# Performance work log

Measured on AMD Instinct MI355X. Metric: run time of the kernel, lower is better.

The kernel has to match this reference:

```python
import jax, jax.numpy as jnp
import numpy as np

N, E, D_IN, HID, HEADS, D_OUT, R = 20000, 640000, 256, 128, 4, 128, 32
NEG_SLOPE = 0.2  # PyG GATConv default


def setup_inputs() -> dict:
    key = jax.random.key(0)
    ks = jax.random.split(key, 12)
    s = 0.05
    return {
        "x": jax.random.normal(ks[0], (N, D_IN), jnp.float32),
        "edge_index": jax.random.randint(ks[1], (2, E), 0, N, dtype=jnp.int64),
        "edge_type": jax.random.randint(ks[2], (E,), 0, R, dtype=jnp.int64),
        "rel_emb": jax.random.normal(ks[3], (R, D_IN), jnp.float32) * s,
        "W1": jax.random.normal(ks[4], (D_IN, HEADS * HID), jnp.float32) * s,
        "att_src1": jax.random.normal(ks[5], (HEADS, HID), jnp.float32) * s,
        "att_dst1": jax.random.normal(ks[6], (HEADS, HID), jnp.float32) * s,
        "b1": jnp.zeros((HEADS * HID,), jnp.float32),
        "W2": jax.random.normal(ks[7], (HEADS * HID, D_OUT), jnp.float32) * s,
        "att_src2": jax.random.normal(ks[8], (1, D_OUT), jnp.float32) * s,
        "att_dst2": jax.random.normal(ks[9], (1, D_OUT), jnp.float32) * s,
        "b2": jnp.zeros((D_OUT,), jnp.float32),
    }


def _gat_conv(x, src, dst, W, a_src, a_dst, bias, heads, ch):
    """PyG GATConv (eval mode, self loops already in src/dst)."""
    n = x.shape[0]
    h = (x @ W).reshape(n, heads, ch)                      # [N,H,C]
    alpha_s = jnp.einsum('nhc,hc->nh', h, a_src)           # [N,H]
    alpha_d = jnp.einsum('nhc,hc->nh', h, a_dst)
    e = jax.nn.leaky_relu(alpha_s[src] + alpha_d[dst], NEG_SLOPE)  # [E,H]
    # segment softmax over incoming edges of each dst node
    m = jax.ops.segment_max(e, dst, num_segments=n)        # [N,H]
    p = jnp.exp(e - m[dst])
    denom = jax.ops.segment_sum(p, dst, num_segments=n)
    alpha = p / (denom[dst] + 1e-16)                       # [E,H]
    out = jax.ops.segment_sum(h[src] * alpha[:, :, None], dst, num_segments=n)
    return out.reshape(n, heads * ch) + bias


def reference(x, edge_index, edge_type, rel_emb, W1, att_src1, att_dst1, b1,
              W2, att_src2, att_dst2, b2):
    src, dst = edge_index[0], edge_index[1]
    # relational feature injection: x_mod[src] += rel_emb[edge_type]
    x_mod = x.at[src].add(rel_emb[edge_type])
    # GATConv adds self loops by default
    loop = jnp.arange(N, dtype=src.dtype)
    s2 = jnp.concatenate([src, loop])
    d2 = jnp.concatenate([dst, loop])
    h = _gat_conv(x_mod, s2, d2, W1, att_src1, att_dst1, b1, HEADS, HID)
    h = jax.nn.elu(h)
    return _gat_conv(h, s2, d2, W2, att_src2, att_dst2, b2, 1, D_OUT)
```

## Files before the change

### kernel.cpp

```cpp
#include <hip/hip_runtime.h>


#define D_IN   256
#define HID1   512
#define NHEADS 4
#define DOUT   128
#define NREL   32
#define NEG_SLOPE 0.2f
#define M_PAD  20096

static __device__ __forceinline__ unsigned short f2b(float f) {
  union { float f; unsigned int i; } v; v.f = f;
  unsigned int x = v.i;
  return (unsigned short)((x + 0x7fffu + ((x >> 16) & 1u)) >> 16);
}
static __device__ __forceinline__ float lrelu(float x) {
  return x > 0.f ? x : NEG_SLOPE * x;
}

typedef __attribute__((ext_vector_type(8))) short bf16x8;
typedef __attribute__((ext_vector_type(4))) float f32x4;
typedef __attribute__((ext_vector_type(2))) float f32x2;

static __device__ __forceinline__ f32x2 up2(unsigned int u) {
  union { unsigned int i; float f; } lo, hi;
  lo.i = u << 16; hi.i = u & 0xffff0000u;
  f32x2 v; v.x = lo.f; v.y = hi.f; return v;
}
static __device__ __forceinline__ void accp(f32x2* acc, float w, uint4 r) {
  f32x2 wv = (f32x2)(w);
  acc[0] += wv * up2(r.x);
  acc[1] += wv * up2(r.y);
  acc[2] += wv * up2(r.z);
  acc[3] += wv * up2(r.w);
}

__global__ void prep_kernel(const int* __restrict__ src, const int* __restrict__ dst,
                            const int* __restrict__ et, int* __restrict__ counts,
                            int* __restrict__ deg, int E, int eb, int cb,
                            const float* __restrict__ W1, const float* __restrict__ W2,
                            unsigned short* __restrict__ W1T, unsigned short* __restrict__ W2T,
                            const float* __restrict__ att_s1, const float* __restrict__ att_d1,
                            float* __restrict__ us4, float* __restrict__ ud4,
                            const float* __restrict__ att_s2, const float* __restrict__ att_d2,
                            float* __restrict__ vs, float* __restrict__ vd) {
  int b = blockIdx.x;
  int t = threadIdx.x;
  if (b < eb) {
    int e = b * 256 + t;
    if (e >= E) return;
    atomicAdd(&counts[(size_t)src[e] * NREL + et[e]], 1);
    atomicAdd(&deg[dst[e]], 1);
  } else if (b < eb + cb) {
    int idx = (b - eb) * 256 + t;
    if (idx < D_IN * HID1) {
      int r = idx / HID1, c = idx % HID1;
      W1T[(size_t)c * D_IN + r] = f2b(W1[idx]);
    } else {
      int k = idx - D_IN * HID1;
      if (k < HID1 * DOUT) {
        int r = k / DOUT, c = k % DOUT;
        W2T[(size_t)c * HID1 + r] = f2b(W2[k]);
      }
    }
  } else if (b == eb + cb) {
    int k = t;
    float us[4] = {0.f, 0.f, 0.f, 0.f}, ud[4] = {0.f, 0.f, 0.f, 0.f};
    for (int h = 0; h < 4; ++h)
      for (int c = 0; c < 128; ++c) {
        float wv = W1[(size_t)k * HID1 + h * 128 + c];
        us[h] += wv * att_s1[h * 128 + c];
        ud[h] += wv * att_d1[h * 128 + c];
      }
    ((float4*)us4)[k] = make_float4(us[0], us[1], us[2], us[3]);
    ((float4*)ud4)[k] = make_float4(ud[0], ud[1], ud[2], ud[3]);
  } else {
#pragma unroll
    for (int rr = 0; rr < 2; ++rr) {
      int r = t * 2 + rr;
      float ss = 0.f, dd = 0.f;
      for (int c = 0; c < DOUT; ++c) {
        float wv = W2[(size_t)r * DOUT + c];
        ss += wv * att_s2[c];
        dd += wv * att_d2[c];
      }
      vs[r] = ss; vd[r] = dd;
    }
  }
}

__global__ void scan_local(const int* __restrict__ in, int* __restrict__ out,
                           int* __restrict__ bsum, int n) {
  __shared__ int wsum[4];
  int t = threadIdx.x;
  int base = blockIdx.x * 1024 + t * 4;
  int v0 = (base + 0 < n) ? in[base + 0] : 0;
  int v1 = (base + 1 < n) ? in[base + 1] : 0;
  int v2 = (base + 2 < n) ? in[base + 2] : 0;
  int v3 = (base + 3 < n) ? in[base + 3] : 0;
  int s = v0 + v1 + v2 + v3;
  int lane = t & 63, w = t >> 6;
  int sc = s;
  for (int off = 1; off < 64; off <<= 1) {
    int u = __shfl_up(sc, off);
    if (lane >= off) sc += u;
  }
  if (lane == 63) wsum[w] = sc;
  __syncthreads();
  int woff = 0;
  for (int i = 0; i < w; ++i) woff += wsum[i];
  int excl = woff + sc - s;
  if (base + 0 < n) out[base + 0] = excl;
  if (base + 1 < n) out[base + 1] = excl + v0;
  if (base + 2 < n) out[base + 2] = excl + v0 + v1;
  if (base + 3 < n) out[base + 3] = excl + v0 + v1 + v2;
  if (t == 255) bsum[blockIdx.x] = woff + sc;
}

__global__ void scan_blocks(int* __restrict__ bsum, int nb,
                            int* __restrict__ offsets, int n) {
  int t = threadIdx.x;
  int v = (t < nb) ? bsum[t] : 0;
  int sc = v;
  for (int off = 1; off < 64; off <<= 1) {
    int u = __shfl_up(sc, off);
    if (t >= off) sc += u;
  }
  if (t < nb) bsum[t] = sc - v;
  if (t == nb - 1) offsets[n] = v;
}

__global__ void scatter_kernel(const int* __restrict__ src, const int* __restrict__ dst,
                               const int* __restrict__ offsets, const int* __restrict__ bsum,
                               int* __restrict__ cursor, int* __restrict__ csr_src, int E) {
  int e = blockIdx.x * 256 + threadIdx.x;
  if (e >= E) return;
  int d = dst[e];
  int pos = offsets[d] + bsum[d >> 10] + atomicAdd(&cursor[d], 1);
  csr_src[pos] = src[e];
}

__global__ __launch_bounds__(256) void xmod_kernel(
    const float* __restrict__ x, const int* __restrict__ counts,
    const float* __restrict__ rel, const float* __restrict__ us4,
    const float* __restrict__ ud4, unsigned short* __restrict__ x_modb,
    float* __restrict__ as1, float* __restrict__ ad1, int n_nodes) {
  int wv = threadIdx.x >> 6;
  int node = blockIdx.x * 4 + wv;
  if (node >= n_nodes) return;
  int l = threadIdx.x & 63;
  int cnt_l = counts[(size_t)node * NREL + (l & 31)];
  const float4* x4 = (const float4*)x;
  const float4* rel4 = (const float4*)rel;
  float4 v = x4[(size_t)node * 64 + l];
#pragma unroll
  for (int r = 0; r < NREL; ++r) {
    int c = __shfl(cnt_l, r);
    if (c) {
      float4 rv = rel4[r * 64 + l];
      float fc = (float)c;
      v.x += fc * rv.x; v.y += fc * rv.y; v.z += fc * rv.z; v.w += fc * rv.w;
    }
  }
  ushort4 o;
  o.x = f2b(v.x); o.y = f2b(v.y); o.z = f2b(v.z); o.w = f2b(v.w);
  *(ushort4*)(x_modb + (size_t)node * D_IN + l * 4) = o;
  const float4* usv = (const float4*)us4;
  const float4* udv = (const float4*)ud4;
  float vv[4] = {v.x, v.y, v.z, v.w};
  float sh[4] = {0.f, 0.f, 0.f, 0.f}, dh[4] = {0.f, 0.f, 0.f, 0.f};
#pragma unroll
  for (int i = 0; i < 4; ++i) {
    float4 uu = usv[l * 4 + i];
    float4 dd = udv[l * 4 + i];
    sh[0] += vv[i] * uu.x; sh[1] += vv[i] * uu.y; sh[2] += vv[i] * uu.z; sh[3] += vv[i] * uu.w;
    dh[0] += vv[i] * dd.x; dh[1] += vv[i] * dd.y; dh[2] += vv[i] * dd.z; dh[3] += vv[i] * dd.w;
  }
  for (int off = 32; off; off >>= 1) {
#pragma unroll
    for (int h = 0; h < 4; ++h) {
      sh[h] += __shfl_xor(sh[h], off);
      dh[h] += __shfl_xor(dh[h], off);
    }
  }
  if (l == 0) {
    ((float4*)as1)[node] = make_float4(sh[0], sh[1], sh[2], sh[3]);
    ((float4*)ad1)[node] = make_float4(dh[0], dh[1], dh[2], dh[3]);
  }
}

__global__ __launch_bounds__(256) void aggregate1_kernel(
    const unsigned short* __restrict__ x_modb,
    const float* __restrict__ as1, const float* __restrict__ ad1,
    const int* __restrict__ offsets, const int* __restrict__ bsum,
    const int* __restrict__ csr_src,
    unsigned short* __restrict__ agg_xb, int n_nodes) {
  int node = blockIdx.x * 4 + (threadIdx.x >> 6);
  if (node >= n_nodes) return;
  int lane = threadIdx.x & 63;
  int hp = lane >> 5, l32 = lane & 31;
  int lo = offsets[node] + bsum[node >> 10];
  int hi = offsets[node + 1] + bsum[(node + 1) >> 10];
  float2 adp = *(const float2*)(ad1 + (size_t)node * 4 + 2 * hp);
  float2 asp = *(const float2*)(as1 + (size_t)node * 4 + 2 * hp);

  const uint4* xv = (const uint4*)x_modb;
  f32x2 acc0[4], acc1[4];
#pragma unroll
  for (int k = 0; k < 4; ++k) { acc0[k] = (f32x2)(0.f); acc1[k] = (f32x2)(0.f); }
  f32x2 den = (f32x2)(0.f);

  int n_it = hi - lo;
  int j = lo;
  int s = (j < hi) ? csr_src[j] : node;
  float2 av = *(const float2*)(as1 + (size_t)s * 4 + 2 * hp);
  for (int i = 0; i < n_it; ++i) {
    int jn = j + 1;
    int sn = (jn < hi) ? csr_src[jn] : node;
    float2 avn = *(const float2*)(as1 + (size_t)sn * 4 + 2 * hp);
    uint4 r = xv[(size_t)s * 32 + l32];
    float w0 = __expf(lrelu(av.x + adp.x));
    float w1 = __expf(lrelu(av.y + adp.y));
    accp(acc0, w0, r);
    accp(acc1, w1, r);
    den.x += w0; den.y += w1;
    j = jn; s = sn; av = avn;
  }
  {
    uint4 r = xv[(size_t)node * 32 + l32];
    float w0 = __expf(lrelu(asp.x + adp.x));
    float w1 = __expf(lrelu(asp.y + adp.y));
    accp(acc0, w0, r);
    accp(acc1, w1, r);
    den.x += w0; den.y += w1;
  }
  float inv0 = 1.f / (den.x + 1e-16f);
  float inv1 = 1.f / (den.y + 1e-16f);
  unsigned int od0[4], od1[4];
#pragma unroll
  for (int p = 0; p < 4; ++p) {
    od0[p] = (unsigned int)f2b(acc0[p].x * inv0) | ((unsigned int)f2b(acc0[p].y * inv0) << 16);
    od1[p] = (unsigned int)f2b(acc1[p].x * inv1) | ((unsigned int)f2b(acc1[p].y * inv1) << 16);
  }
  uint4 o0; o0.x = od0[0]; o0.y = od0[1]; o0.z = od0[2]; o0.w = od0[3];
  uint4 o1; o1.x = od1[0]; o1.y = od1[1]; o1.z = od1[2]; o1.w = od1[3];
  *(uint4*)(agg_xb + ((size_t)(2 * hp) * M_PAD + node) * D_IN + l32 * 8) = o0;
  *(uint4*)(agg_xb + ((size_t)(2 * hp + 1) * M_PAD + node) * D_IN + l32 * 8) = o1;
}

template <int BM, int MODE>
__global__ __launch_bounds__(256) void mfma_gemm(
    const unsigned short* __restrict__ A, const unsigned short* __restrict__ BT,
    unsigned short* __restrict__ C, int M, int N, int K,
    const float* __restrict__ bias, const float* __restrict__ vs,
    const float* __restrict__ vd, float* __restrict__ as2, float* __restrict__ ad2) {
  constexpr int MFR = BM / 32;
  __shared__ __align__(16) unsigned short Asl[BM * 32];
  __shared__ __align__(16) unsigned short Bsl[128 * 32];
  int tid = threadIdx.x;
  int m0 = blockIdx.y * BM, n0 = blockIdx.x * 128;
  int lane = tid & 63, wv = tid >> 6;
  int wm = wv & 1, wn = wv >> 1;
  int l16 = lane & 15, quad = lane >> 4;
  int lr = lane >> 2, lseg = lane & 3;
  if (MODE == 1) A += (size_t)blockIdx.x * M_PAD * K;

  f32x4 acc[MFR][4];
#pragma unroll
  for (int i = 0; i < MFR; ++i)
#pragma unroll
    for (int j = 0; j < 4; ++j) acc[i][j] = (f32x4)(0.f);

  for (int k0 = 0; k0 < K; k0 += 32) {
#pragma unroll
    for (int c = wv; c < BM / 16; c += 4) {
      int gr = m0 + c * 16 + lr; gr = gr < M ? gr : M - 1;
      __builtin_amdgcn_global_load_lds(
          (const __attribute__((address_space(1))) void*)(A + (size_t)gr * K + k0 + lseg * 8),
          (__attribute__((address_space(3))) void*)(&Asl[c * 512]), 16, 0, 0);
    }
#pragma unroll
    for (int c = wv; c < 8; c += 4) {
      int gr = n0 + c * 16 + lr;
      __builtin_amdgcn_global_load_lds(
          (const __attribute__((address_space(1))) void*)(BT + (size_t)gr * K + k0 + lseg * 8),
          (__attribute__((address_space(3))) void*)(&Bsl[c * 512]), 16, 0, 0);
    }
    __syncthreads();
    bf16x8 af[MFR], bfr[4];
#pragma unroll
    for (int mf = 0; mf < MFR; ++mf)
      af[mf] = *(const bf16x8*)(&Asl[(wm * (BM / 2) + mf * 16 + l16) * 32 + quad * 8]);
#pragma unroll
    for (int nf = 0; nf < 4; ++nf)
      bfr[nf] = *(const bf16x8*)(&Bsl[(wn * 64 + nf * 16 + l16) * 32 + quad * 8]);
#pragma unroll
    for (int mf = 0; mf < MFR; ++mf)
#pragma unroll
      for (int nf = 0; nf < 4; ++nf)
        acc[mf][nf] = __builtin_amdgcn_mfma_f32_16x16x32_bf16(af[mf], bfr[nf], acc[mf][nf], 0, 0, 0);
    __syncthreads();
  }
  if (MODE == 0) {
#pragma unroll
    for (int mf = 0; mf < MFR; ++mf)
#pragma unroll
      for (int nf = 0; nf < 4; ++nf)
#pragma unroll
        for (int r = 0; r < 4; ++r) {
          int row = m0 + wm * (BM / 2) + mf * 16 + quad * 4 + r;
          int col = n0 + wn * 64 + nf * 16 + l16;
          C[(size_t)row * N + col] = f2b(acc[mf][nf][r]);
        }
  } else {
#pragma unroll
    for (int mf = 0; mf < MFR; ++mf)
#pragma unroll
      for (int r = 0; r < 4; ++r) {
        int row = m0 + wm * (BM / 2) + mf * 16 + quad * 4 + r;
        float sd = 0.f, dd = 0.f;
#pragma unroll
        for (int nf = 0; nf < 4; ++nf) {
          int col = n0 + wn * 64 + nf * 16 + l16;
          float cv = acc[mf][nf][r] + bias[col];
          cv = cv > 0.f ? cv : expm1f(cv);
          C[(size_t)row * N + col] = f2b(cv);
          sd += cv * vs[col];
          dd += cv * vd[col];
        }
#pragma unroll
        for (int off = 1; off < 16; off <<= 1) {
          sd += __shfl_xor(sd, off);
          dd += __shfl_xor(dd, off);
        }
        if (l16 == 0 && row < M) {
          atomicAdd(&as2[row], sd);
          atomicAdd(&ad2[row], dd);
        }
      }
  }
}

__global__ __launch_bounds__(256) void aggregate2_kernel(
    const unsigned short* __restrict__ t2b,
    const float* __restrict__ as2, const float* __restrict__ ad2,
    const int* __restrict__ offsets, const int* __restrict__ bsum,
    const int* __restrict__ csr_src,
    const float* __restrict__ bias, float* __restrict__ out, int n_nodes) {
  int node = blockIdx.x * 4 + (threadIdx.x >> 6);
  if (node >= n_nodes) return;
  int lane = threadIdx.x & 63;
  int g = lane >> 4, l16 = lane & 15;
  int lo = offsets[node] + bsum[node >> 10];
  int hi = offsets[node + 1] + bsum[(node + 1) >> 10];
  float ad = ad2[node];

  const uint4* t2v = (const uint4*)t2b;
  f32x2 acc[4];
#pragma unroll
  for (int k = 0; k < 4; ++k) acc[k] = (f32x2)(0.f);
  float denom = 0.f;
  int nit = (hi - lo + 3) >> 2;
  int j = lo + g;
  bool valid = j < hi;
  int s = valid ? csr_src[j] : node;
  float asv = as2[s];
  for (int i = 0; i < nit; ++i) {
    int jn = j + 4;
    bool vn = jn < hi;
    int sn = vn ? csr_src[jn] : node;
    float asv_n = as2[sn];
    uint4 tv = t2v[(size_t)s * 16 + l16];
    float w = valid ? __expf(lrelu(asv + ad)) : 0.f;
    accp(acc, w, tv);
    denom += w;
    j = jn; valid = vn; s = sn; asv = asv_n;
  }
  if (g == 0) {
    uint4 tv = t2v[(size_t)node * 16 + l16];
    float w = __expf(lrelu(as2[node] + ad));
    accp(acc, w, tv);
    denom += w;
  }
#pragma unroll
  for (int k = 0; k < 4; ++k) {
    acc[k].x += __shfl_xor(acc[k].x, 16); acc[k].y += __shfl_xor(acc[k].y, 16);
    acc[k].x += __shfl_xor(acc[k].x, 32); acc[k].y += __shfl_xor(acc[k].y, 32);
  }
  denom += __shfl_xor(denom, 16);
  denom += __shfl_xor(denom, 32);
  if (g == 0) {
    float inv = 1.f / (denom + 1e-16f);
    float4 o0, o1;
    o0.x = acc[0].x * inv + bias[l16 * 8 + 0];
    o0.y = acc[0].y * inv + bias[l16 * 8 + 1];
    o0.z = acc[1].x * inv + bias[l16 * 8 + 2];
    o0.w = acc[1].y * inv + bias[l16 * 8 + 3];
    o1.x = acc[2].x * inv + bias[l16 * 8 + 4];
    o1.y = acc[2].y * inv + bias[l16 * 8 + 5];
    o1.z = acc[3].x * inv + bias[l16 * 8 + 6];
    o1.w = acc[3].y * inv + bias[l16 * 8 + 7];
    *(float4*)(out + (size_t)node * DOUT + l16 * 8) = o0;
    *(float4*)(out + (size_t)node * DOUT + l16 * 8 + 4) = o1;
  }
}

extern "C" void kernel_launch(void* const* d_in, const int* in_sizes, int n_in,
                              void* d_out, int out_size, void* d_ws, size_t ws_size,
                              hipStream_t stream) {
  const float* x     = (const float*)d_in[0];
  const int* ei      = (const int*)d_in[1];
  const int* etype   = (const int*)d_in[2];
  const float* rel   = (const float*)d_in[3];
  const float* W1    = (const float*)d_in[4];
  const float* at_s1 = (const float*)d_in[5];
  const float* at_d1 = (const float*)d_in[6];
  const float* b1    = (const float*)d_in[7];
  const float* W2    = (const float*)d_in[8];
  const float* at_s2 = (const float*)d_in[9];
  const float* at_d2 = (const float*)d_in[10];
  const float* b2v   = (const float*)d_in[11];
  float* out         = (float*)d_out;

  const int N = in_sizes[0] / D_IN;
  const int E = in_sizes[2];
  const int* srcv = ei;
  const int* dstv = ei + E;

  char* p = (char*)d_ws;
  auto carve = [&](size_t bytes) -> char* {
    char* r = p; p += (bytes + 255) & ~(size_t)255; return r;
  };
  int*   counts  = (int*)carve((size_t)N * NREL * 4);
  int*   deg     = (int*)carve((size_t)N * 4);
  int*   offsets = (int*)carve(((size_t)N + 1) * 4);
  int*   cursor  = (int*)carve((size_t)N * 4);
  int*   bsum    = (int*)carve(64 * 4);
  float* as2     = (float*)carve((size_t)N * 4);
  float* ad2     = (float*)carve((size_t)N * 4);
  size_t zero_bytes = (size_t)(p - (char*)counts);
  float* as1     = (float*)carve((size_t)N * NHEADS * 4);
  float* ad1     = (float*)carve((size_t)N * NHEADS * 4);
  float* vs      = (float*)carve((size_t)HID1 * 4);
  float* vd      = (float*)carve((size_t)HID1 * 4);
  float* us4     = (float*)carve((size_t)D_IN * 4 * 4);
  float* ud4     = (float*)carve((size_t)D_IN * 4 * 4);
  int*   csr_src = (int*)carve((size_t)E * 4);
  unsigned short* W1T    = (unsigned short*)carve((size_t)HID1 * D_IN * 2);
  unsigned short* W2T    = (unsigned short*)carve((size_t)DOUT * HID1 * 2);
  unsigned short* x_modb = (unsigned short*)carve((size_t)N * D_IN * 2);
  unsigned short* agg_xb = (unsigned short*)carve((size_t)NHEADS * M_PAD * D_IN * 2);
  unsigned short* h2b    = (unsigned short*)carve((size_t)M_PAD * HID1 * 2);
  unsigned short* t2b    = (unsigned short*)carve((size_t)M_PAD * DOUT * 2);

  hipMemsetAsync(counts, 0, zero_bytes, stream);

  int eb = (E + 255) / 256;
  int cb = (D_IN * HID1 + HID1 * DOUT + 255) / 256;
  int nb = (N + 1023) / 1024;
  prep_kernel<<<eb + cb + 2, 256, 0, stream>>>(srcv, dstv, etype, counts, deg, E, eb, cb,
                                               W1, W2, W1T, W2T, at_s1, at_d1, us4, ud4,
                                               at_s2, at_d2, vs, vd);
  scan_local<<<nb, 256, 0, stream>>>(deg, offsets, bsum, N);
  scan_blocks<<<1, 64, 0, stream>>>(bsum, nb, offsets, N);
  scatter_kernel<<<eb, 256, 0, stream>>>(srcv, dstv, offsets, bsum, cursor, csr_src, E);
  xmod_kernel<<<(N + 3) / 4, 256, 0, stream>>>(x, counts, rel, us4, ud4, x_modb, as1, ad1, N);
  aggregate1_kernel<<<(N + 3) / 4, 256, 0, stream>>>(x_modb, as1, ad1, offsets, bsum,
                                                     csr_src, agg_xb, N);
  mfma_gemm<128, 1><<<dim3(NHEADS, M_PAD / 128), 256, 0, stream>>>(
      agg_xb, W1T, h2b, N, HID1, D_IN, b1, vs, vd, as2, ad2);
  mfma_gemm<64, 0><<<dim3(DOUT / 128, M_PAD / 64), 256, 0, stream>>>(
      h2b, W2T, t2b, N, DOUT, HID1, nullptr, nullptr, nullptr, nullptr, nullptr);
  aggregate2_kernel<<<(N + 3) / 4, 256, 0, stream>>>(
      t2b, as2, ad2, offsets, bsum, csr_src, b2v, out, N);
}
```

Measured before the change: 344.1 us.

## Build CSR with per-block LDS histograms and restructure layer-1 aggregation loop

Replaces global-atomic degree counting and scatter with 128 blocks that each build an LDS histogram of destinations, followed by column-sum, rebase and LDS-cursor scatter kernels. Packs relation counts into 8-bit fields to shrink the counts buffer and its atomics. Rewrites aggregate1 so each half-wave handles alternate edges for all four heads using packed FMA asm with a prefetch of the next row, and adds row prefetching to aggregate2. Risks: 8-bit counts overflow if a node has more than 255 edges of one relation, the new scatter order is deterministic but extra kernel launches are added, and the gtable aliases the h2b buffer.

```diff
diff --git a/kernel.cpp b/kernel.cpp
--- a/kernel.cpp
+++ b/kernel.cpp
@@ -8,6 +8,7 @@
 #define NREL   32
 #define NEG_SLOPE 0.2f
 #define M_PAD  20096
+#define NB     128
 
 static __device__ __forceinline__ unsigned short f2b(float f) {
   union { float f; unsigned int i; } v; v.f = f;
@@ -27,32 +28,67 @@
   lo.i = u << 16; hi.i = u & 0xffff0000u;
   f32x2 v; v.x = lo.f; v.y = hi.f; return v;
 }
+static __device__ __forceinline__ void pkfma(f32x2& a, f32x2 b, f32x2 c) {
+  asm("v_pk_fma_f32 %0, %1, %2, %0" : "+v"(a) : "v"(b), "v"(c));
+}
 static __device__ __forceinline__ void accp(f32x2* acc, float w, uint4 r) {
   f32x2 wv = (f32x2)(w);
-  acc[0] += wv * up2(r.x);
-  acc[1] += wv * up2(r.y);
-  acc[2] += wv * up2(r.z);
-  acc[3] += wv * up2(r.w);
-}
-
-__global__ void prep_kernel(const int* __restrict__ src, const int* __restrict__ dst,
-                            const int* __restrict__ et, int* __restrict__ counts,
-                            int* __restrict__ deg, int E, int eb, int cb,
-                            const float* __restrict__ W1, const float* __restrict__ W2,
-                            unsigned short* __restrict__ W1T, unsigned short* __restrict__ W2T,
-                            const float* __restrict__ att_s1, const float* __restrict__ att_d1,
-                            float* __restrict__ us4, float* __restrict__ ud4,
-                            const float* __restrict__ att_s2, const float* __restrict__ att_d2,
-                            float* __restrict__ vs, float* __restrict__ vd) {
+  pkfma(acc[0], wv, up2(r.x));
+  pkfma(acc[1], wv, up2(r.y));
+  pkfma(acc[2], wv, up2(r.z));
+  pkfma(acc[3], wv, up2(r.w));
+}
+static __device__ __forceinline__ void acc4(f32x2 acc[4][4], float* den,
+                                            float4 av, float4 adv, uint4 r) {
+  float w0 = __expf(lrelu(av.x + adv.x));
+  float w1 = __expf(lrelu(av.y + adv.y));
+  float w2 = __expf(lrelu(av.z + adv.z));
+  float w3 = __expf(lrelu(av.w + adv.w));
+  f32x2 x0 = up2(r.x), x1 = up2(r.y), x2 = up2(r.z), x3 = up2(r.w);
+  f32x2 wv;
+  wv = (f32x2)(w0);
+  pkfma(acc[0][0], wv, x0); pkfma(acc[0][1], wv, x1);
+  pkfma(acc[0][2], wv, x2); pkfma(acc[0][3], wv, x3);
+  wv = (f32x2)(w1);
+  pkfma(acc[1][0], wv, x0); pkfma(acc[1][1], wv, x1);
+  pkfma(acc[1][2], wv, x2); pkfma(acc[1][3], wv, x3);
+  wv = (f32x2)(w2);
+  pkfma(acc[2][0], wv, x0); pkfma(acc[2][1], wv, x1);
+  pkfma(acc[2][2], wv, x2); pkfma(acc[2][3], wv, x3);
+  wv = (f32x2)(w3);
+  pkfma(acc[3][0], wv, x0); pkfma(acc[3][1], wv, x1);
+  pkfma(acc[3][2], wv, x2); pkfma(acc[3][3], wv, x3);
+  den[0] += w0; den[1] += w1; den[2] += w2; den[3] += w3;
+}
+
+__global__ __launch_bounds__(256) void hist_prep_kernel(
+    const int* __restrict__ src, const int* __restrict__ dst,
+    const int* __restrict__ et, unsigned int* __restrict__ counts8,
+    int* __restrict__ gtable, int E, int n, int cb,
+    const float* __restrict__ W1, const float* __restrict__ W2,
+    unsigned short* __restrict__ W1T, unsigned short* __restrict__ W2T,
+    const float* __restrict__ att_s1, const float* __restrict__ att_d1,
+    float* __restrict__ us4, float* __restrict__ ud4,
+    const float* __restrict__ att_s2, const float* __restrict__ att_d2,
+    float* __restrict__ vs, float* __restrict__ vd) {
   int b = blockIdx.x;
   int t = threadIdx.x;
-  if (b < eb) {
-    int e = b * 256 + t;
-    if (e >= E) return;
-    atomicAdd(&counts[(size_t)src[e] * NREL + et[e]], 1);
-    atomicAdd(&deg[dst[e]], 1);
-  } else if (b < eb + cb) {
-    int idx = (b - eb) * 256 + t;
+  if (b < NB) {
+    extern __shared__ int hist[];
+    for (int i = t; i < n; i += 256) hist[i] = 0;
+    __syncthreads();
+    int per = (E + NB - 1) / NB;
+    int e0 = b * per;
+    int e1 = min(e0 + per, E);
+    for (int e = e0 + t; e < e1; e += 256) {
+      atomicAdd(&hist[dst[e]], 1);
+      int s = src[e], r = et[e];
+      atomicAdd(&counts8[(size_t)s * 8 + (r >> 2)], 1u << (8 * (r & 3)));
+    }
+    __syncthreads();
+    for (int i = t; i < n; i += 256) gtable[(size_t)b * n + i] = hist[i];
+  } else if (b < NB + cb) {
+    int idx = (b - NB) * 256 + t;
     if (idx < D_IN * HID1) {
       int r = idx / HID1, c = idx % HID1;
       W1T[(size_t)c * D_IN + r] = f2b(W1[idx]);
@@ -63,7 +99,7 @@
         W2T[(size_t)c * HID1 + r] = f2b(W2[k]);
       }
     }
-  } else if (b == eb + cb) {
+  } else if (b == NB + cb) {
     int k = t;
     float us[4] = {0.f, 0.f, 0.f, 0.f}, ud[4] = {0.f, 0.f, 0.f, 0.f};
     for (int h = 0; h < 4; ++h)
@@ -87,6 +123,16 @@
       vs[r] = ss; vd[r] = dd;
     }
   }
+}
+
+__global__ void colsum_kernel(const int* __restrict__ gtable,
+                              int* __restrict__ deg, int n) {
+  int d = blockIdx.x * 256 + threadIdx.x;
+  if (d >= n) return;
+  int s = 0;
+#pragma unroll 8
+  for (int b = 0; b < NB; ++b) s += gtable[(size_t)b * n + d];
+  deg[d] = s;
 }
 
 __global__ void scan_local(const int* __restrict__ in, int* __restrict__ out,
@@ -130,18 +176,39 @@
   if (t == nb - 1) offsets[n] = v;
 }
 
-__global__ void scatter_kernel(const int* __restrict__ src, const int* __restrict__ dst,
-                               const int* __restrict__ offsets, const int* __restrict__ bsum,
-                               int* __restrict__ cursor, int* __restrict__ csr_src, int E) {
-  int e = blockIdx.x * 256 + threadIdx.x;
-  if (e >= E) return;
-  int d = dst[e];
-  int pos = offsets[d] + bsum[d >> 10] + atomicAdd(&cursor[d], 1);
-  csr_src[pos] = src[e];
+__global__ void rebase_kernel(int* __restrict__ gtable,
+                              const int* __restrict__ offsets,
+                              const int* __restrict__ bsum, int n) {
+  int d = blockIdx.x * 256 + threadIdx.x;
+  if (d >= n) return;
+  int run = offsets[d] + bsum[d >> 10];
+  for (int b = 0; b < NB; ++b) {
+    size_t idx = (size_t)b * n + d;
+    int v = gtable[idx];
+    gtable[idx] = run;
+    run += v;
+  }
+}
+
+__global__ __launch_bounds__(256) void scatter2_kernel(
+    const int* __restrict__ src, const int* __restrict__ dst,
+    const int* __restrict__ gtable, int* __restrict__ csr_src, int E, int n) {
+  extern __shared__ int cur[];
+  int b = blockIdx.x;
+  int t = threadIdx.x;
+  for (int i = t; i < n; i += 256) cur[i] = gtable[(size_t)b * n + i];
+  __syncthreads();
+  int per = (E + NB - 1) / NB;
+  int e0 = b * per;
+  int e1 = min(e0 + per, E);
+  for (int e = e0 + t; e < e1; e += 256) {
+    int pos = atomicAdd(&cur[dst[e]], 1);
+    csr_src[pos] = src[e];
+  }
 }
 
 __global__ __launch_bounds__(256) void xmod_kernel(
-    const float* __restrict__ x, const int* __restrict__ counts,
+    const float* __restrict__ x, const unsigned int* __restrict__ counts8,
     const float* __restrict__ rel, const float* __restrict__ us4,
     const float* __restrict__ ud4, unsigned short* __restrict__ x_modb,
     float* __restrict__ as1, float* __restrict__ ad1, int n_nodes) {
@@ -149,7 +216,9 @@
   int node = blockIdx.x * 4 + wv;
   if (node >= n_nodes) return;
   int l = threadIdx.x & 63;
-  int cnt_l = counts[(size_t)node * NREL + (l & 31)];
+  int r5 = l & 31;
+  unsigned int cw = counts8[(size_t)node * 8 + (r5 >> 2)];
+  int cnt_l = (int)((cw >> (8 * (r5 & 3))) & 0xffu);
   const float4* x4 = (const float4*)x;
   const float4* rel4 = (const float4*)rel;
   float4 v = x4[(size_t)node * 64 + l];
@@ -198,54 +267,58 @@
   int node = blockIdx.x * 4 + (threadIdx.x >> 6);
   if (node >= n_nodes) return;
   int lane = threadIdx.x & 63;
-  int hp = lane >> 5, l32 = lane & 31;
+  int half = lane >> 5, l32 = lane & 31;
   int lo = offsets[node] + bsum[node >> 10];
   int hi = offsets[node + 1] + bsum[(node + 1) >> 10];
-  float2 adp = *(const float2*)(ad1 + (size_t)node * 4 + 2 * hp);
-  float2 asp = *(const float2*)(as1 + (size_t)node * 4 + 2 * hp);
-
+  float4 adv = ((const float4*)ad1)[node];
   const uint4* xv = (const uint4*)x_modb;
-  f32x2 acc0[4], acc1[4];
-#pragma unroll
-  for (int k = 0; k < 4; ++k) { acc0[k] = (f32x2)(0.f); acc1[k] = (f32x2)(0.f); }
-  f32x2 den = (f32x2)(0.f);
-
-  int n_it = hi - lo;
-  int j = lo;
+  const float4* as1v = (const float4*)as1;
+
+  f32x2 acc[4][4];
+#pragma unroll
+  for (int h = 0; h < 4; ++h)
+#pragma unroll
+    for (int k = 0; k < 4; ++k) acc[h][k] = (f32x2)(0.f);
+  float den[4] = {0.f, 0.f, 0.f, 0.f};
+
+  int j = lo + half;
   int s = (j < hi) ? csr_src[j] : node;
-  float2 av = *(const float2*)(as1 + (size_t)s * 4 + 2 * hp);
-  for (int i = 0; i < n_it; ++i) {
-    int jn = j + 1;
+  float4 av = as1v[(unsigned)s];
+  uint4 r = xv[(unsigned)((s << 5) | l32)];
+  while (j < hi) {
+    int jn = j + 2;
     int sn = (jn < hi) ? csr_src[jn] : node;
-    float2 avn = *(const float2*)(as1 + (size_t)sn * 4 + 2 * hp);
-    uint4 r = xv[(size_t)s * 32 + l32];
-    float w0 = __expf(lrelu(av.x + adp.x));
-    float w1 = __expf(lrelu(av.y + adp.y));
-    accp(acc0, w0, r);
-    accp(acc1, w1, r);
-    den.x += w0; den.y += w1;
-    j = jn; s = sn; av = avn;
-  }
-  {
-    uint4 r = xv[(size_t)node * 32 + l32];
-    float w0 = __expf(lrelu(asp.x + adp.x));
-    float w1 = __expf(lrelu(asp.y + adp.y));
-    accp(acc0, w0, r);
-    accp(acc1, w1, r);
-    den.x += w0; den.y += w1;
-  }
-  float inv0 = 1.f / (den.x + 1e-16f);
-  float inv1 = 1.f / (den.y + 1e-16f);
-  unsigned int od0[4], od1[4];
-#pragma unroll
-  for (int p = 0; p < 4; ++p) {
-    od0[p] = (unsigned int)f2b(acc0[p].x * inv0) | ((unsigned int)f2b(acc0[p].y * inv0) << 16);
-    od1[p] = (unsigned int)f2b(acc1[p].x * inv1) | ((unsigned int)f2b(acc1[p].y * inv1) << 16);
-  }
-  uint4 o0; o0.x = od0[0]; o0.y = od0[1]; o0.z = od0[2]; o0.w = od0[3];
-  uint4 o1; o1.x = od1[0]; o1.y = od1[1]; o1.z = od1[2]; o1.w = od1[3];
-  *(uint4*)(agg_xb + ((size_t)(2 * hp) * M_PAD + node) * D_IN + l32 * 8) = o0;
-  *(uint4*)(agg_xb + ((size_t)(2 * hp + 1) * M_PAD + node) * D_IN + l32 * 8) = o1;
+    float4 avn = as1v[(unsigned)sn];
+    uint4 rn = xv[(unsigned)((sn << 5) | l32)];
+    acc4(acc, den, av, adv, r);
+    j = jn; s = sn; av = avn; r = rn;
+  }
+  if (half == 0) {
+    float4 asv = as1v[(unsigned)node];
+    uint4 rs = xv[(unsigned)((node << 5) | l32)];
+    acc4(acc, den, asv, adv, rs);
+  }
+#pragma unroll
+  for (int h = 0; h < 4; ++h) {
+#pragma unroll
+    for (int k = 0; k < 4; ++k) {
+      acc[h][k].x += __shfl_xor(acc[h][k].x, 32);
+      acc[h][k].y += __shfl_xor(acc[h][k].y, 32);
+    }
+    den[h] += __shfl_xor(den[h], 32);
+  }
+  if (half == 0) {
+#pragma unroll
+    for (int h = 0; h < 4; ++h) {
+      float inv = 1.f / (den[h] + 1e-16f);
+      uint4 o;
+      o.x = (unsigned)f2b(acc[h][0].x * inv) | ((unsigned)f2b(acc[h][0].y * inv) << 16);
+      o.y = (unsigned)f2b(acc[h][1].x * inv) | ((unsigned)f2b(acc[h][1].y * inv) << 16);
+      o.z = (unsigned)f2b(acc[h][2].x * inv) | ((unsigned)f2b(acc[h][2].y * inv) << 16);
+      o.w = (unsigned)f2b(acc[h][3].x * inv) | ((unsigned)f2b(acc[h][3].y * inv) << 16);
+      *(uint4*)(agg_xb + ((size_t)h * M_PAD + node) * D_IN + l32 * 8) = o;
+    }
+  }
 }
 
 template <int BM, int MODE>
@@ -365,21 +438,22 @@
   bool valid = j < hi;
   int s = valid ? csr_src[j] : node;
   float asv = as2[s];
+  uint4 tv = t2v[(unsigned)((s << 4) | l16)];
   for (int i = 0; i < nit; ++i) {
     int jn = j + 4;
     bool vn = jn < hi;
     int sn = vn ? csr_src[jn] : node;
     float asv_n = as2[sn];
-    uint4 tv = t2v[(size_t)s * 16 + l16];
+    uint4 tvn = t2v[(unsigned)((sn << 4) | l16)];
     float w = valid ? __expf(lrelu(asv + ad)) : 0.f;
     accp(acc, w, tv);
     denom += w;
-    j = jn; valid = vn; s = sn; asv = asv_n;
+    j = jn; valid = vn; s = sn; asv = asv_n; tv = tvn;
   }
   if (g == 0) {
-    uint4 tv = t2v[(size_t)node * 16 + l16];
+    uint4 tv2 = t2v[(unsigned)((node << 4) | l16)];
     float w = __expf(lrelu(as2[node] + ad));
-    accp(acc, w, tv);
+    accp(acc, w, tv2);
     denom += w;
   }
 #pragma unroll
@@ -431,14 +505,13 @@
   auto carve = [&](size_t bytes) -> char* {
     char* r = p; p += (bytes + 255) & ~(size_t)255; return r;
   };
-  int*   counts  = (int*)carve((size_t)N * NREL * 4);
+  unsigned int* counts8 = (unsigned int*)carve((size_t)N * 8 * 4);
+  float* as2     = (float*)carve((size_t)N * 4);
+  float* ad2     = (float*)carve((size_t)N * 4);
+  size_t zero_bytes = (size_t)(p - (char*)counts8);
   int*   deg     = (int*)carve((size_t)N * 4);
   int*   offsets = (int*)carve(((size_t)N + 1) * 4);
-  int*   cursor  = (int*)carve((size_t)N * 4);
   int*   bsum    = (int*)carve(64 * 4);
-  float* as2     = (float*)carve((size_t)N * 4);
-  float* ad2     = (float*)carve((size_t)N * 4);
-  size_t zero_bytes = (size_t)(p - (char*)counts);
   float* as1     = (float*)carve((size_t)N * NHEADS * 4);
   float* ad1     = (float*)carve((size_t)N * NHEADS * 4);
   float* vs      = (float*)carve((size_t)HID1 * 4);
@@ -452,19 +525,22 @@
   unsigned short* agg_xb = (unsigned short*)carve((size_t)NHEADS * M_PAD * D_IN * 2);
   unsigned short* h2b    = (unsigned short*)carve((size_t)M_PAD * HID1 * 2);
   unsigned short* t2b    = (unsigned short*)carve((size_t)M_PAD * DOUT * 2);
-
-  hipMemsetAsync(counts, 0, zero_bytes, stream);
-
-  int eb = (E + 255) / 256;
+  int* gtable = (int*)h2b;
+
+  hipMemsetAsync(counts8, 0, zero_bytes, stream);
+
   int cb = (D_IN * HID1 + HID1 * DOUT + 255) / 256;
   int nb = (N + 1023) / 1024;
-  prep_kernel<<<eb + cb + 2, 256, 0, stream>>>(srcv, dstv, etype, counts, deg, E, eb, cb,
-                                               W1, W2, W1T, W2T, at_s1, at_d1, us4, ud4,
-                                               at_s2, at_d2, vs, vd);
+  int ldsb = N * 4;
+  hist_prep_kernel<<<NB + cb + 2, 256, ldsb, stream>>>(
+      srcv, dstv, etype, counts8, gtable, E, N, cb,
+      W1, W2, W1T, W2T, at_s1, at_d1, us4, ud4, at_s2, at_d2, vs, vd);
+  colsum_kernel<<<(N + 255) / 256, 256, 0, stream>>>(gtable, deg, N);
   scan_local<<<nb, 256, 0, stream>>>(deg, offsets, bsum, N);
   scan_blocks<<<1, 64, 0, stream>>>(bsum, nb, offsets, N);
-  scatter_kernel<<<eb, 256, 0, stream>>>(srcv, dstv, offsets, bsum, cursor, csr_src, E);
-  xmod_kernel<<<(N + 3) / 4, 256, 0, stream>>>(x, counts, rel, us4, ud4, x_modb, as1, ad1, N);
+  rebase_kernel<<<(N + 255) / 256, 256, 0, stream>>>(gtable, offsets, bsum, N);
+  scatter2_kernel<<<NB, 256, ldsb, stream>>>(srcv, dstv, gtable, csr_src, E, N);
+  xmod_kernel<<<(N + 3) / 4, 256, 0, stream>>>(x, counts8, rel, us4, ud4, x_modb, as1, ad1, N);
   aggregate1_kernel<<<(N + 3) / 4, 256, 0, stream>>>(x_modb, as1, ad1, offsets, bsum,
                                                      csr_src, agg_xb, N);
   mfma_gemm<128, 1><<<dim3(NHEADS, M_PAD / 128), 256, 0, stream>>>(
```

After: 306.0 us. 11.1% less time.
